# Performance work log

Hardware: AMD Instinct MI355X
Metric: run time of the kernel (lower is better)

## Reference

```python
import jax, jax.numpy as jnp
import numpy as np

N_POINTS = 131072  # 32 clouds * 4096 points
N_SEG = 32


def setup_inputs() -> dict:
    key = jax.random.key(0)
    ks = jax.random.split(key, 8)
    x = jax.random.normal(ks[0], (N_POINTS, 256), dtype=jnp.float32)
    pos = jax.random.normal(ks[1], (N_POINTS, 3), dtype=jnp.float32)
    # sorted segment ids, every segment non-empty (equal-size clouds)
    batch = jnp.repeat(jnp.arange(N_SEG, dtype=jnp.int32), N_POINTS // N_SEG)
    def lin(k, fan_in, fan_out):
        s = 1.0 / np.sqrt(fan_in)
        return jax.random.uniform(k, (fan_in, fan_out), jnp.float32, -s, s)
    W1 = lin(ks[2], 259, 256); b1 = jnp.zeros((256,), jnp.float32)
    W2 = lin(ks[3], 256, 512); b2 = jnp.zeros((512,), jnp.float32)
    W3 = lin(ks[4], 512, 1024); b3 = jnp.zeros((1024,), jnp.float32)
    return {"x": x, "pos": pos, "batch": batch,
            "W1": W1, "b1": b1, "W2": W2, "b2": b2, "W3": W3, "b3": b3}


def reference(x, pos, batch, W1, b1, W2, b2, W3, b3):
    # concat point features with coordinates: [N, 256+3]
    h = jnp.concatenate([x, pos], axis=1)
    # shared point-wise MLP (Linear + ReLU per layer)
    h = jax.nn.relu(h @ W1 + b1)   # [N, 256]
    h = jax.nn.relu(h @ W2 + b2)   # [N, 512]
    h = jax.nn.relu(h @ W3 + b3)   # [N, 1024]
    # global_max_pool: batch-indexed segment max -> [N_SEG, 1024]
    return jax.ops.segment_max(h, batch, num_segments=N_SEG)
```

## Files before the change

kernel.cpp:

```cpp
#include <hip/hip_runtime.h>
#include <stdint.h>

typedef unsigned short ushort_t;
typedef short shortx8 __attribute__((ext_vector_type(8)));
typedef float floatx4 __attribute__((ext_vector_type(4)));
typedef unsigned short ushortx8 __attribute__((ext_vector_type(8)));

__device__ __forceinline__ unsigned short f2bf(float f) {
  union { float f; unsigned int u; } v; v.f = f;
  unsigned int u = v.u;
  return (unsigned short)((u + 0x7fffu + ((u >> 16) & 1u)) >> 16);
}

__device__ __forceinline__ void gload_lds16(const void* g, void* l) {
  __builtin_amdgcn_global_load_lds(
      (const __attribute__((address_space(1))) unsigned int*)g,
      (__attribute__((address_space(3))) unsigned int*)l, 16, 0, 0);
}

__global__ void prep_w_k(const float* __restrict__ W1, const float* __restrict__ W2,
                         const float* __restrict__ W3, ushort_t* __restrict__ W1T,
                         ushort_t* __restrict__ W2T, ushort_t* __restrict__ W3T) {
  int idx = blockIdx.x * blockDim.x + threadIdx.x;
  const float* in; ushort_t* out; int K, N;
  if (idx < 256 * 256)                  { in = W1; out = W1T; K = 256; N = 256; }
  else if (idx < 256 * 256 + 512 * 256) { idx -= 256 * 256; in = W2; out = W2T; K = 256; N = 512; }
  else if (idx < 256 * 256 + 512 * 256 + 1024 * 512) {
    idx -= 256 * 256 + 512 * 256; in = W3; out = W3T; K = 512; N = 1024;
  } else return;
  int n = idx / K, k = idx - n * K;
  out[idx] = f2bf(in[k * N + n]);
}

template <int K, int NOUT, int MODE>
__global__ __launch_bounds__(256, 2) void gemm_kernel(
    const ushort_t* __restrict__ A, const ushort_t* __restrict__ BT,
    const float* __restrict__ bias, ushort_t* __restrict__ C,
    const float* __restrict__ pos, const float* __restrict__ W1tail,
    float* __restrict__ pool, const float* __restrict__ Afp) {
  __shared__ __align__(16) ushort_t As[128 * 64];
  __shared__ __align__(16) ushort_t Bs[128 * 64];

  const int m0 = blockIdx.x * 128;
  const int n0 = blockIdx.y * 128;
  const int tid = threadIdx.x;
  const int w = tid >> 6;
  const int l = tid & 63;
  const int wm = w >> 1, wn = w & 1;
  const int lane16 = l & 15, lq = l >> 4;
  const int s7 = lane16 & 7;

  const int srow = l >> 3;
  const int sg = (l & 7) ^ srow;

  floatx4 acc[4][4] = {};

  for (int k0 = 0; k0 < K; k0 += 64) {
    if (MODE == 1) {
#pragma unroll
      for (int rep = 0; rep < 4; ++rep) {
        const int g = rep * 256 + tid;
        const int row = g >> 3, slot = g & 7;
        const int sgr = slot ^ (row & 7);
        const float4* src = (const float4*)(Afp + (size_t)(m0 + row) * K + k0 + sgr * 8);
        float4 a = src[0], b = src[1];
        ushortx8 v;
        v[0] = f2bf(a.x); v[1] = f2bf(a.y); v[2] = f2bf(a.z); v[3] = f2bf(a.w);
        v[4] = f2bf(b.x); v[5] = f2bf(b.y); v[6] = f2bf(b.z); v[7] = f2bf(b.w);
        *(ushortx8*)(As + row * 64 + slot * 8) = v;
      }
    } else {
#pragma unroll
      for (int r = 0; r < 4; ++r) {
        const int c = r * 4 + w;
        const int row = c * 8 + srow;
        gload_lds16(A + (size_t)(m0 + row) * K + k0 + sg * 8, As + c * 512);
      }
    }
#pragma unroll
    for (int r = 0; r < 4; ++r) {
      const int c = r * 4 + w;
      const int row = c * 8 + srow;
      gload_lds16(BT + (size_t)(n0 + row) * K + k0 + sg * 8, Bs + c * 512);
    }
    __syncthreads();
#pragma unroll
    for (int kk = 0; kk < 2; ++kk) {
      shortx8 af[4], bfr[4];
#pragma unroll
      for (int i = 0; i < 4; ++i) {
        const int row = wm * 64 + i * 16 + lane16;
        af[i] = *(const shortx8*)(As + row * 64 + ((kk * 4 + lq) ^ s7) * 8);
      }
#pragma unroll
      for (int j = 0; j < 4; ++j) {
        const int row = wn * 64 + j * 16 + lane16;
        bfr[j] = *(const shortx8*)(Bs + row * 64 + ((kk * 4 + lq) ^ s7) * 8);
      }
#pragma unroll
      for (int i = 0; i < 4; ++i)
#pragma unroll
        for (int j = 0; j < 4; ++j)
          acc[i][j] = __builtin_amdgcn_mfma_f32_16x16x32_bf16(af[i], bfr[j], acc[i][j], 0, 0, 0);
    }
    __syncthreads();
  }

  float bv[4];
#pragma unroll
  for (int j = 0; j < 4; ++j) bv[j] = bias[n0 + wn * 64 + j * 16 + lane16];

  if (MODE == 2) {
    const int seg = m0 >> 12;
#pragma unroll
    for (int j = 0; j < 4; ++j) {
      float vmax = 0.0f;
#pragma unroll
      for (int i = 0; i < 4; ++i)
#pragma unroll
        for (int r = 0; r < 4; ++r) vmax = fmaxf(vmax, acc[i][j][r] + bv[j]);
      vmax = fmaxf(vmax, __shfl_xor(vmax, 16, 64));
      vmax = fmaxf(vmax, __shfl_xor(vmax, 32, 64));
      if (l < 16) {
        int n = n0 + wn * 64 + j * 16 + lane16;
        atomicMax((int*)(pool + (size_t)seg * NOUT + n), __float_as_int(vmax));
      }
    }
  } else {
#pragma unroll
    for (int i = 0; i < 4; ++i) {
#pragma unroll
      for (int r = 0; r < 4; ++r) {
        int m = m0 + wm * 64 + i * 16 + lq * 4 + r;
        float p0 = 0.f, p1 = 0.f, p2 = 0.f;
        if (MODE == 1) { p0 = pos[m * 3 + 0]; p1 = pos[m * 3 + 1]; p2 = pos[m * 3 + 2]; }
#pragma unroll
        for (int j = 0; j < 4; ++j) {
          int n = n0 + wn * 64 + j * 16 + lane16;
          float v = acc[i][j][r] + bv[j];
          if (MODE == 1) v += p0 * W1tail[n] + p1 * W1tail[256 + n] + p2 * W1tail[512 + n];
          v = fmaxf(v, 0.0f);
          C[(size_t)m * NOUT + n] = f2bf(v);
        }
      }
    }
  }
}


extern "C" void kernel_launch(void* const* d_in, const int* in_sizes, int n_in,
                              void* d_out, int out_size, void* d_ws, size_t ws_size,
                              hipStream_t stream) {
  const float* x   = (const float*)d_in[0];
  const float* pos = (const float*)d_in[1];
  const float* W1 = (const float*)d_in[3];
  const float* b1 = (const float*)d_in[4];
  const float* W2 = (const float*)d_in[5];
  const float* b2 = (const float*)d_in[6];
  const float* W3 = (const float*)d_in[7];
  const float* b3 = (const float*)d_in[8];
  float* out = (float*)d_out;

  const int M = in_sizes[0] / 256;

  char* ws = (char*)d_ws;
  ushort_t* H2  = (ushort_t*)ws;
  ushort_t* H1  = (ushort_t*)(ws + (size_t)M * 512 * 2);
  ushort_t* W1T = (ushort_t*)(ws + (size_t)M * 512 * 2 + (size_t)M * 256 * 2);
  ushort_t* W2T = W1T + 256 * 256;
  ushort_t* W3T = W2T + 512 * 256;

  const int ntr = 256 * 256 + 512 * 256 + 1024 * 512;
  prep_w_k<<<(ntr + 255) / 256, 256, 0, stream>>>(W1, W2, W3, W1T, W2T, W3T);

  gemm_kernel<256, 256, 1><<<dim3(M / 128, 2), 256, 0, stream>>>(
      nullptr, W1T, b1, H1, pos, W1 + 256 * 256, nullptr, x);
  gemm_kernel<256, 512, 0><<<dim3(M / 128, 4), 256, 0, stream>>>(
      H1, W2T, b2, H2, nullptr, nullptr, nullptr, nullptr);
  gemm_kernel<512, 1024, 2><<<dim3(M / 128, 8), 256, 0, stream>>>(
      H2, W3T, b3, nullptr, nullptr, nullptr, out, nullptr);
}
```

Baseline: 451.6 us.

## Double-buffer LDS tiles with register prefetch in GEMM main loop

Replaces the direct global-to-LDS loads and the two barriers per k-step with a register-staged, double-buffered pipeline. The next k-tile is loaded into registers before the MFMA work on the current LDS buffer, then written to the alternate buffer, leaving one barrier per iteration. The goal is to hide global load latency behind the matrix math. In exchange LDS use doubles to 64KB per block and register pressure rises, which could reduce occupancy under launch_bounds(256,2).

```diff
diff --git a/kernel.cpp b/kernel.cpp
--- a/kernel.cpp
+++ b/kernel.cpp
@@ -10,12 +10,6 @@
   union { float f; unsigned int u; } v; v.f = f;
   unsigned int u = v.u;
   return (unsigned short)((u + 0x7fffu + ((u >> 16) & 1u)) >> 16);
-}
-
-__device__ __forceinline__ void gload_lds16(const void* g, void* l) {
-  __builtin_amdgcn_global_load_lds(
-      (const __attribute__((address_space(1))) unsigned int*)g,
-      (__attribute__((address_space(3))) unsigned int*)l, 16, 0, 0);
 }
 
 __global__ void prep_w_k(const float* __restrict__ W1, const float* __restrict__ W2,
@@ -38,8 +32,8 @@
     const float* __restrict__ bias, ushort_t* __restrict__ C,
     const float* __restrict__ pos, const float* __restrict__ W1tail,
     float* __restrict__ pool, const float* __restrict__ Afp) {
-  __shared__ __align__(16) ushort_t As[128 * 64];
-  __shared__ __align__(16) ushort_t Bs[128 * 64];
+  __shared__ __align__(16) ushort_t As[2][128 * 64];
+  __shared__ __align__(16) ushort_t Bs[2][128 * 64];
 
   const int m0 = blockIdx.x * 128;
   const int n0 = blockIdx.y * 128;
@@ -50,60 +44,92 @@
   const int lane16 = l & 15, lq = l >> 4;
   const int s7 = lane16 & 7;
 
-  const int srow = l >> 3;
-  const int sg = (l & 7) ^ srow;
+  const int srow = tid >> 3;
+  const int slot = tid & 7;
+  const int sg = slot ^ (srow & 7);
 
   floatx4 acc[4][4] = {};
-
-  for (int k0 = 0; k0 < K; k0 += 64) {
+  constexpr int NIT = K / 64;
+
+  ushortx8 aR[4], bR[4];
+  float4 aF[4][2];
+
+#pragma unroll
+  for (int rep = 0; rep < 4; ++rep) {
+    const int row = rep * 32 + srow;
     if (MODE == 1) {
+      const float4* src = (const float4*)(Afp + (size_t)(m0 + row) * K + sg * 8);
+      aF[rep][0] = src[0]; aF[rep][1] = src[1];
+    } else {
+      aR[rep] = *(const ushortx8*)(A + (size_t)(m0 + row) * K + sg * 8);
+    }
+    bR[rep] = *(const ushortx8*)(BT + (size_t)(n0 + row) * K + sg * 8);
+  }
+#pragma unroll
+  for (int rep = 0; rep < 4; ++rep) {
+    const int row = rep * 32 + srow;
+    ushortx8 av;
+    if (MODE == 1) {
+      float4 a = aF[rep][0], b = aF[rep][1];
+      av[0] = f2bf(a.x); av[1] = f2bf(a.y); av[2] = f2bf(a.z); av[3] = f2bf(a.w);
+      av[4] = f2bf(b.x); av[5] = f2bf(b.y); av[6] = f2bf(b.z); av[7] = f2bf(b.w);
+    } else av = aR[rep];
+    *(ushortx8*)(&As[0][row * 64 + slot * 8]) = av;
+    *(ushortx8*)(&Bs[0][row * 64 + slot * 8]) = bR[rep];
+  }
+  __syncthreads();
+
+#pragma unroll
+  for (int it = 0; it < NIT; ++it) {
+    const int cur = it & 1, nxt = cur ^ 1;
+    if (it + 1 < NIT) {
+      const int k0 = (it + 1) * 64;
 #pragma unroll
       for (int rep = 0; rep < 4; ++rep) {
-        const int g = rep * 256 + tid;
-        const int row = g >> 3, slot = g & 7;
-        const int sgr = slot ^ (row & 7);
-        const float4* src = (const float4*)(Afp + (size_t)(m0 + row) * K + k0 + sgr * 8);
-        float4 a = src[0], b = src[1];
-        ushortx8 v;
-        v[0] = f2bf(a.x); v[1] = f2bf(a.y); v[2] = f2bf(a.z); v[3] = f2bf(a.w);
-        v[4] = f2bf(b.x); v[5] = f2bf(b.y); v[6] = f2bf(b.z); v[7] = f2bf(b.w);
-        *(ushortx8*)(As + row * 64 + slot * 8) = v;
-      }
-    } else {
-#pragma unroll
-      for (int r = 0; r < 4; ++r) {
-        const int c = r * 4 + w;
-        const int row = c * 8 + srow;
-        gload_lds16(A + (size_t)(m0 + row) * K + k0 + sg * 8, As + c * 512);
-      }
-    }
-#pragma unroll
-    for (int r = 0; r < 4; ++r) {
-      const int c = r * 4 + w;
-      const int row = c * 8 + srow;
-      gload_lds16(BT + (size_t)(n0 + row) * K + k0 + sg * 8, Bs + c * 512);
-    }
-    __syncthreads();
+        const int row = rep * 32 + srow;
+        if (MODE == 1) {
+          const float4* src = (const float4*)(Afp + (size_t)(m0 + row) * K + k0 + sg * 8);
+          aF[rep][0] = src[0]; aF[rep][1] = src[1];
+        } else {
+          aR[rep] = *(const ushortx8*)(A + (size_t)(m0 + row) * K + k0 + sg * 8);
+        }
+        bR[rep] = *(const ushortx8*)(BT + (size_t)(n0 + row) * K + k0 + sg * 8);
+      }
+    }
 #pragma unroll
     for (int kk = 0; kk < 2; ++kk) {
-      shortx8 af[4], bfr[4];
+      shortx8 af[4], bfv[4];
 #pragma unroll
       for (int i = 0; i < 4; ++i) {
         const int row = wm * 64 + i * 16 + lane16;
-        af[i] = *(const shortx8*)(As + row * 64 + ((kk * 4 + lq) ^ s7) * 8);
+        af[i] = *(const shortx8*)(&As[cur][row * 64 + ((kk * 4 + lq) ^ s7) * 8]);
       }
 #pragma unroll
       for (int j = 0; j < 4; ++j) {
         const int row = wn * 64 + j * 16 + lane16;
-        bfr[j] = *(const shortx8*)(Bs + row * 64 + ((kk * 4 + lq) ^ s7) * 8);
+        bfv[j] = *(const shortx8*)(&Bs[cur][row * 64 + ((kk * 4 + lq) ^ s7) * 8]);
       }
 #pragma unroll
       for (int i = 0; i < 4; ++i)
 #pragma unroll
         for (int j = 0; j < 4; ++j)
-          acc[i][j] = __builtin_amdgcn_mfma_f32_16x16x32_bf16(af[i], bfr[j], acc[i][j], 0, 0, 0);
-    }
-    __syncthreads();
+          acc[i][j] = __builtin_amdgcn_mfma_f32_16x16x32_bf16(af[i], bfv[j], acc[i][j], 0, 0, 0);
+    }
+    if (it + 1 < NIT) {
+#pragma unroll
+      for (int rep = 0; rep < 4; ++rep) {
+        const int row = rep * 32 + srow;
+        ushortx8 av;
+        if (MODE == 1) {
+          float4 a = aF[rep][0], b = aF[rep][1];
+          av[0] = f2bf(a.x); av[1] = f2bf(a.y); av[2] = f2bf(a.z); av[3] = f2bf(a.w);
+          av[4] = f2bf(b.x); av[5] = f2bf(b.y); av[6] = f2bf(b.z); av[7] = f2bf(b.w);
+        } else av = aR[rep];
+        *(ushortx8*)(&As[nxt][row * 64 + slot * 8]) = av;
+        *(ushortx8*)(&Bs[nxt][row * 64 + slot * 8]) = bR[rep];
+      }
+      __syncthreads();
+    }
   }
 
   float bv[4];
```

After: 498.3 us. +10.3%, slower.
